# Kernel optimization log

Hardware: AMD Instinct MI355X
Metric: run time of the kernel (lower is better)

The kernel has to match this reference:

```python
import jax, jax.numpy as jnp
import numpy as np

B, T, D, H, S = 32, 2048, 512, 64, 3  # batch, time, feature_dim, flow hidden, flow steps
NBLK = 2  # nflows MADE default num_blocks
LOG_2PI = np.float32(np.log(2.0 * np.pi))


def setup_inputs() -> dict:
    key = jax.random.key(0)
    ks = jax.random.split(key, 20)
    rn = lambda k, sh: jax.random.normal(k, sh, dtype=jnp.float32) * 0.05
    return {
        "trend": rn(ks[0], (B, T)),
        "seasonal": rn(ks[1], (B, T)),
        "residual": rn(ks[2], (B, T)),
        # Linear(1, D) for trend / seasonal
        "Wt": rn(ks[3], (D, 1)), "bt": rn(ks[4], (D,)),
        "Ws": rn(ks[5], (D, 1)), "bs": rn(ks[6], (D,)),
        # per-flow-step MADE params (stacked over S steps). With features=1 the
        # masked initial layer contributes only its bias.
        "b_init": rn(ks[7], (S, H)),
        "Wc0": rn(ks[8], (S, H, 1)), "bc0": rn(ks[9], (S, H)),
        # two residual blocks per step: lin1, lin2, context gate
        "W1": rn(ks[10], (S, NBLK, H, H)), "b1": rn(ks[11], (S, NBLK, H)),
        "W2": rn(ks[12], (S, NBLK, H, H)), "b2": rn(ks[13], (S, NBLK, H)),
        "Wcb": rn(ks[14], (S, NBLK, H, 1)), "bcb": rn(ks[15], (S, NBLK, H)),
        # final Linear(H, 2): (unconstrained_scale, shift)
        "Wf": rn(ks[16], (S, 2, H)), "bf": rn(ks[17], (S, 2)),
    }


def _flow_log_prob(x, c, b_init, Wc0, bc0, W1, b1, W2, b2, Wcb, bcb, Wf, bf):
    # x: [N] residual values, c: [N,1] context (previous residual)
    z = x
    logdet = jnp.zeros_like(x)
    for i in range(S):
        h = c @ Wc0[i].T + (bc0[i] + b_init[i])  # [N,H]; input path is fully masked (features=1)
        for j in range(NBLK):  # MaskedResidualBlock
            t = jax.nn.relu(h) @ W1[i, j].T + b1[i, j]
            t = jax.nn.relu(t) @ W2[i, j].T + b2[i, j]
            g = c @ Wcb[i, j].T + bcb[i, j]
            h = h + t * jax.nn.sigmoid(g)  # F.glu(cat(t, g))
        out = jax.nn.relu(h) @ Wf[i].T + bf[i]  # [N,2]
        scale = jax.nn.softplus(out[:, 0]) + 1e-3
        z = scale * z + out[:, 1]
        logdet = logdet + jnp.log(scale)
    return -0.5 * z * z - 0.5 * LOG_2PI + logdet  # StandardNormal.log_prob + logabsdet


def reference(trend, seasonal, residual, Wt, bt, Ws, bs, b_init, Wc0, bc0,
              W1, b1, W2, b2, Wcb, bcb, Wf, bf):
    # Linear(1, D): y = x * W[:,0] + b
    feat_trend = trend[..., None] * Wt[:, 0] + bt      # [B,T,D]
    feat_seasonal = seasonal[..., None] * Ws[:, 0] + bs  # [B,T,D]
    x = residual.reshape(-1)                            # [B*T]
    prev = jnp.concatenate([jnp.zeros_like(residual[:, :1]), residual[:, :-1]], axis=1)
    c = prev.reshape(-1, 1)                             # [B*T,1]
    lp = _flow_log_prob(x, c, b_init, Wc0, bc0, W1, b1, W2, b2, Wcb, bcb, Wf, bf)
    lp = jax.lax.stop_gradient(lp).reshape(B, T, 1)     # torch.no_grad()
    return jnp.concatenate([feat_trend, feat_seasonal, lp], axis=-1)  # [B,T,2D+1]
```

## Files before the change

### kernel.cpp

```cpp
#include <hip/hip_runtime.h>

#define NB 32
#define NT 2048
#define ND 512
#define NH 64
#define NS 3
#define NBLKS 2
#define ROWLEN (2*ND + 1)

typedef __attribute__((ext_vector_type(8))) short bf16x8;
typedef float f32x4 __attribute__((ext_vector_type(4)));

#define W1_OFF 0
#define W2_OFF 24576
#define WF_OFF 49152
#define WS_ELEMS 52224

__device__ __forceinline__ unsigned int f2bf(float f) {
    unsigned int u = __float_as_uint(f);
    return (u + 0x7FFFu + ((u >> 16) & 1u)) >> 16;
}
__device__ __forceinline__ unsigned int pack2(float a, float b) {
    return f2bf(a) | (f2bf(b) << 16);
}

__global__ __launch_bounds__(256) void prepack(
    const float* __restrict__ W1, const float* __restrict__ W2,
    const float* __restrict__ Wf, unsigned short* __restrict__ ws)
{
    int idx = blockIdx.x * 256 + threadIdx.x;
    if (idx < 24576) {
        ws[W1_OFF + idx] = (unsigned short)f2bf(W1[idx]);
    } else if (idx < 49152) {
        int o = idx - 24576;
        ws[W2_OFF + o] = (unsigned short)f2bf(W2[o]);
    } else if (idx < WS_ELEMS) {
        int o = idx - 49152;
        int s = o >> 10, row = (o >> 6) & 15, m = o & 63;
        float v = (row < 2) ? Wf[s * 128 + row * 64 + m] : 0.0f;
        ws[WF_OFF + o] = (unsigned short)f2bf(v);
    }
}

__global__ __launch_bounds__(256, 4) void nf_main(
    const float* __restrict__ trend, const float* __restrict__ seasonal,
    const float* __restrict__ residual,
    const float* __restrict__ Wt, const float* __restrict__ bt,
    const float* __restrict__ Ws, const float* __restrict__ bs,
    const float* __restrict__ b_init, const float* __restrict__ Wc0,
    const float* __restrict__ bc0,
    const float* __restrict__ b1, const float* __restrict__ b2,
    const float* __restrict__ Wcb, const float* __restrict__ bcb,
    const float* __restrict__ bf_, const unsigned short* __restrict__ wpk,
    float* __restrict__ out)
{
    __shared__ float s_tr[64], s_se[64];
    __shared__ unsigned short s_X[4][16][72];

    const int tid  = threadIdx.x;
    const int row0 = blockIdx.x * 64;

    if (tid < 64) { s_tr[tid] = trend[row0 + tid]; s_se[tid] = seasonal[row0 + tid]; }
    __syncthreads();

    {
        float wv[4], bv[4];
        #pragma unroll
        for (int j = 0; j < 4; ++j) {
            int cc = tid + 256 * j;
            if (cc < ND) { wv[j] = Wt[cc];      bv[j] = bt[cc]; }
            else         { wv[j] = Ws[cc - ND]; bv[j] = bs[cc - ND]; }
        }
        for (int rr = 0; rr < 64; ++rr) {
            float a = s_tr[rr], sv = s_se[rr];
            float* rp = out + (size_t)(row0 + rr) * ROWLEN;
            #pragma unroll
            for (int j = 0; j < 4; ++j) {
                int cc = tid + 256 * j;
                rp[cc] = fmaf((cc < ND) ? a : sv, wv[j], bv[j]);
            }
        }
    }

    const int lane = tid & 63;
    const int wv_  = tid >> 6;
    const int r    = lane & 15;
    const int q    = lane >> 4;
    const int n    = row0 + wv_ * 16 + r;
    const float x  = residual[n];
    const float c  = ((n & (NT - 1)) == 0) ? 0.0f : residual[n - 1];
    unsigned short (* const X)[72] = s_X[wv_];
    const int u0 = 4 * q;

    float z = x, logdet = 0.0f;

    for (int i = 0; i < NS; ++i) {
        float h[4][4];
        #pragma unroll
        for (int t = 0; t < 4; ++t) {
            const int ub = i * NH + 16 * t + u0;
            const f32x4 wc  = *(const f32x4*)(Wc0 + ub);
            const f32x4 b0v = *(const f32x4*)(bc0 + ub);
            const f32x4 biv = *(const f32x4*)(b_init + ub);
            #pragma unroll
            for (int e = 0; e < 4; ++e) h[t][e] = fmaf(c, wc[e], b0v[e] + biv[e]);
        }

        for (int j = 0; j < NBLKS; ++j) {
            const int ij = i * NBLKS + j;
            #pragma unroll
            for (int t = 0; t < 4; ++t) {
                uint2 p;
                p.x = pack2(fmaxf(h[t][0], 0.f), fmaxf(h[t][1], 0.f));
                p.y = pack2(fmaxf(h[t][2], 0.f), fmaxf(h[t][3], 0.f));
                *(uint2*)&X[r][16 * t + u0] = p;
            }
            __syncthreads();

            f32x4 D[4];
            {
                const unsigned short* Wb = wpk + W1_OFF + ij * 4096;
                bf16x8 bA = *(const bf16x8*)&X[r][8 * q];
                bf16x8 bB = *(const bf16x8*)&X[r][32 + 8 * q];
                #pragma unroll
                for (int t = 0; t < 4; ++t) {
                    bf16x8 a0 = *(const bf16x8*)&Wb[(16 * t + r) * 64 + 8 * q];
                    bf16x8 a1 = *(const bf16x8*)&Wb[(16 * t + r) * 64 + 32 + 8 * q];
                    f32x4 d = {0.f, 0.f, 0.f, 0.f};
                    d = __builtin_amdgcn_mfma_f32_16x16x32_bf16(a0, bA, d, 0, 0, 0);
                    d = __builtin_amdgcn_mfma_f32_16x16x32_bf16(a1, bB, d, 0, 0, 0);
                    D[t] = d;
                }
            }
            #pragma unroll
            for (int t = 0; t < 4; ++t) {
                const f32x4 bb = *(const f32x4*)(b1 + ij * NH + 16 * t + u0);
                uint2 p;
                p.x = pack2(fmaxf(D[t][0] + bb[0], 0.f), fmaxf(D[t][1] + bb[1], 0.f));
                p.y = pack2(fmaxf(D[t][2] + bb[2], 0.f), fmaxf(D[t][3] + bb[3], 0.f));
                *(uint2*)&X[r][16 * t + u0] = p;
            }
            __syncthreads();

            {
                const unsigned short* Wb = wpk + W2_OFF + ij * 4096;
                bf16x8 bA = *(const bf16x8*)&X[r][8 * q];
                bf16x8 bB = *(const bf16x8*)&X[r][32 + 8 * q];
                #pragma unroll
                for (int t = 0; t < 4; ++t) {
                    bf16x8 a0 = *(const bf16x8*)&Wb[(16 * t + r) * 64 + 8 * q];
                    bf16x8 a1 = *(const bf16x8*)&Wb[(16 * t + r) * 64 + 32 + 8 * q];
                    f32x4 d = {0.f, 0.f, 0.f, 0.f};
                    d = __builtin_amdgcn_mfma_f32_16x16x32_bf16(a0, bA, d, 0, 0, 0);
                    d = __builtin_amdgcn_mfma_f32_16x16x32_bf16(a1, bB, d, 0, 0, 0);
                    D[t] = d;
                }
            }
            #pragma unroll
            for (int t = 0; t < 4; ++t) {
                const int ub = ij * NH + 16 * t + u0;
                const f32x4 b2v = *(const f32x4*)(b2 + ub);
                const f32x4 wg  = *(const f32x4*)(Wcb + ub);
                const f32x4 bg  = *(const f32x4*)(bcb + ub);
                #pragma unroll
                for (int e = 0; e < 4; ++e) {
                    float g  = fmaf(c, wg[e], bg[e]);
                    float sg = 1.0f / (1.0f + __expf(-g));
                    h[t][e] += (D[t][e] + b2v[e]) * sg;
                }
            }
        }

        #pragma unroll
        for (int t = 0; t < 4; ++t) {
            uint2 p;
            p.x = pack2(fmaxf(h[t][0], 0.f), fmaxf(h[t][1], 0.f));
            p.y = pack2(fmaxf(h[t][2], 0.f), fmaxf(h[t][3], 0.f));
            *(uint2*)&X[r][16 * t + u0] = p;
        }
        __syncthreads();
        {
            const unsigned short* Wb = wpk + WF_OFF + i * 1024;
            bf16x8 bA = *(const bf16x8*)&X[r][8 * q];
            bf16x8 bB = *(const bf16x8*)&X[r][32 + 8 * q];
            bf16x8 a0 = *(const bf16x8*)&Wb[r * 64 + 8 * q];
            bf16x8 a1 = *(const bf16x8*)&Wb[r * 64 + 32 + 8 * q];
            f32x4 d = {0.f, 0.f, 0.f, 0.f};
            d = __builtin_amdgcn_mfma_f32_16x16x32_bf16(a0, bA, d, 0, 0, 0);
            d = __builtin_amdgcn_mfma_f32_16x16x32_bf16(a1, bB, d, 0, 0, 0);
            float o0 = d[0] + bf_[2 * i];
            float o1 = d[1] + bf_[2 * i + 1];
            float sp = log1pf(__expf(o0)) + 1e-3f;
            z = fmaf(sp, z, o1);
            logdet += __logf(sp);
        }
        __syncthreads();
    }

    if (q == 0)
        out[(size_t)n * ROWLEN + 2 * ND] = fmaf(-0.5f, z * z, logdet) - 0.91893853320467274178f;
}

extern "C" void kernel_launch(void* const* d_in, const int* in_sizes, int n_in,
                              void* d_out, int out_size, void* d_ws, size_t ws_size,
                              hipStream_t stream) {
    const float* trend    = (const float*)d_in[0];
    const float* seasonal = (const float*)d_in[1];
    const float* residual = (const float*)d_in[2];
    const float* Wt       = (const float*)d_in[3];
    const float* bt       = (const float*)d_in[4];
    const float* Ws       = (const float*)d_in[5];
    const float* bs       = (const float*)d_in[6];
    const float* b_init   = (const float*)d_in[7];
    const float* Wc0      = (const float*)d_in[8];
    const float* bc0      = (const float*)d_in[9];
    const float* W1       = (const float*)d_in[10];
    const float* b1       = (const float*)d_in[11];
    const float* W2       = (const float*)d_in[12];
    const float* b2       = (const float*)d_in[13];
    const float* Wcb      = (const float*)d_in[14];
    const float* bcb      = (const float*)d_in[15];
    const float* Wf       = (const float*)d_in[16];
    const float* bfin     = (const float*)d_in[17];
    float* out            = (float*)d_out;
    unsigned short* wpk   = (unsigned short*)d_ws;

    hipLaunchKernelGGL(prepack, dim3(WS_ELEMS / 256), dim3(256), 0, stream, W1, W2, Wf, wpk);

    const int nrows = NB * NT;
    hipLaunchKernelGGL(nf_main, dim3(nrows / 64), dim3(256), 0, stream,
                       trend, seasonal, residual, Wt, bt, Ws, bs,
                       b_init, Wc0, bc0, b1, b2, Wcb, bcb, bfin, wpk, out);
}
```

Baseline: 355.3 us.

## Replace block barriers with wave-level syncs and move feature writes after flow

Each wave only touches its own slice of the shared staging buffer, so the block-wide __syncthreads are replaced with wavefront-scoped fences and wave barriers, and extra wave syncs guard the write-after-read hazards. The Linear(1,D) feature write moves from a block-level loop staged through shared memory to a per-wave loop after the flow computation. That loop broadcasts each row's trend and seasonal value with readlane, so the feature stores can overlap other waves' MFMA work. The launch-bounds occupancy hint drops from 4 to 2, which may raise register use. The feature-weight arrays grow to 16 registers per lane.

```diff
diff --git a/kernel.cpp b/kernel.cpp
--- a/kernel.cpp
+++ b/kernel.cpp
@@ -22,6 +22,16 @@
 }
 __device__ __forceinline__ unsigned int pack2(float a, float b) {
     return f2bf(a) | (f2bf(b) << 16);
+}
+
+__device__ __forceinline__ void wave_sync() {
+    __builtin_amdgcn_fence(__ATOMIC_ACQ_REL, "wavefront");
+    __builtin_amdgcn_wave_barrier();
+    __builtin_amdgcn_fence(__ATOMIC_ACQ_REL, "wavefront");
+}
+
+__device__ __forceinline__ float bcast(float v, int l) {
+    return __int_as_float(__builtin_amdgcn_readlane(__float_as_int(v), l));
 }
 
 __global__ __launch_bounds__(256) void prepack(
@@ -42,7 +52,7 @@
     }
 }
 
-__global__ __launch_bounds__(256, 4) void nf_main(
+__global__ __launch_bounds__(256, 2) void nf_main(
     const float* __restrict__ trend, const float* __restrict__ seasonal,
     const float* __restrict__ residual,
     const float* __restrict__ Wt, const float* __restrict__ bt,
@@ -54,41 +64,21 @@
     const float* __restrict__ bf_, const unsigned short* __restrict__ wpk,
     float* __restrict__ out)
 {
-    __shared__ float s_tr[64], s_se[64];
     __shared__ unsigned short s_X[4][16][72];
 
     const int tid  = threadIdx.x;
     const int row0 = blockIdx.x * 64;
-
-    if (tid < 64) { s_tr[tid] = trend[row0 + tid]; s_se[tid] = seasonal[row0 + tid]; }
-    __syncthreads();
-
-    {
-        float wv[4], bv[4];
-        #pragma unroll
-        for (int j = 0; j < 4; ++j) {
-            int cc = tid + 256 * j;
-            if (cc < ND) { wv[j] = Wt[cc];      bv[j] = bt[cc]; }
-            else         { wv[j] = Ws[cc - ND]; bv[j] = bs[cc - ND]; }
-        }
-        for (int rr = 0; rr < 64; ++rr) {
-            float a = s_tr[rr], sv = s_se[rr];
-            float* rp = out + (size_t)(row0 + rr) * ROWLEN;
-            #pragma unroll
-            for (int j = 0; j < 4; ++j) {
-                int cc = tid + 256 * j;
-                rp[cc] = fmaf((cc < ND) ? a : sv, wv[j], bv[j]);
-            }
-        }
-    }
-
     const int lane = tid & 63;
     const int wv_  = tid >> 6;
     const int r    = lane & 15;
     const int q    = lane >> 4;
     const int n    = row0 + wv_ * 16 + r;
-    const float x  = residual[n];
-    const float c  = ((n & (NT - 1)) == 0) ? 0.0f : residual[n - 1];
+
+    const float x   = residual[n];
+    const float c   = ((n & (NT - 1)) == 0) ? 0.0f : residual[n - 1];
+    const float trv = trend[n];
+    const float sev = seasonal[n];
+
     unsigned short (* const X)[72] = s_X[wv_];
     const int u0 = 4 * q;
 
@@ -115,7 +105,7 @@
                 p.y = pack2(fmaxf(h[t][2], 0.f), fmaxf(h[t][3], 0.f));
                 *(uint2*)&X[r][16 * t + u0] = p;
             }
-            __syncthreads();
+            wave_sync();
 
             f32x4 D[4];
             {
@@ -132,6 +122,7 @@
                     D[t] = d;
                 }
             }
+            wave_sync();
             #pragma unroll
             for (int t = 0; t < 4; ++t) {
                 const f32x4 bb = *(const f32x4*)(b1 + ij * NH + 16 * t + u0);
@@ -140,7 +131,7 @@
                 p.y = pack2(fmaxf(D[t][2] + bb[2], 0.f), fmaxf(D[t][3] + bb[3], 0.f));
                 *(uint2*)&X[r][16 * t + u0] = p;
             }
-            __syncthreads();
+            wave_sync();
 
             {
                 const unsigned short* Wb = wpk + W2_OFF + ij * 4096;
@@ -169,6 +160,7 @@
                     h[t][e] += (D[t][e] + b2v[e]) * sg;
                 }
             }
+            wave_sync();
         }
 
         #pragma unroll
@@ -178,7 +170,7 @@
             p.y = pack2(fmaxf(h[t][2], 0.f), fmaxf(h[t][3], 0.f));
             *(uint2*)&X[r][16 * t + u0] = p;
         }
-        __syncthreads();
+        wave_sync();
         {
             const unsigned short* Wb = wpk + WF_OFF + i * 1024;
             bf16x8 bA = *(const bf16x8*)&X[r][8 * q];
@@ -194,11 +186,29 @@
             z = fmaf(sp, z, o1);
             logdet += __logf(sp);
         }
-        __syncthreads();
+        wave_sync();
     }
 
     if (q == 0)
         out[(size_t)n * ROWLEN + 2 * ND] = fmaf(-0.5f, z * z, logdet) - 0.91893853320467274178f;
+
+    float wv[16], bv[16];
+    #pragma unroll
+    for (int j = 0; j < 16; ++j) {
+        const int cc = lane + 64 * j;
+        wv[j] = (j < 8) ? Wt[cc] : Ws[cc - ND];
+        bv[j] = (j < 8) ? bt[cc] : bs[cc - ND];
+    }
+    const int rbase = row0 + wv_ * 16;
+    #pragma unroll
+    for (int j = 0; j < 16; ++j) {
+        const int cc = lane + 64 * j;
+        const float src = (j < 8) ? trv : sev;
+        #pragma unroll
+        for (int rr = 0; rr < 16; ++rr) {
+            out[(size_t)(rbase + rr) * ROWLEN + cc] = fmaf(bcast(src, rr), wv[j], bv[j]);
+        }
+    }
 }
 
 extern "C" void kernel_launch(void* const* d_in, const int* in_sizes, int n_in,
@@ -225,7 +235,8 @@
     float* out            = (float*)d_out;
     unsigned short* wpk   = (unsigned short*)d_ws;
 
-    hipLaunchKernelGGL(prepack, dim3(WS_ELEMS / 256), dim3(256), 0, stream, W1, W2, Wf, wpk);
+    hipLaunchKernelGGL(prepack, dim3((WS_ELEMS + 255) / 256), dim3(256), 0, stream,
+                       W1, W2, Wf, wpk);
 
     const int nrows = NB * NT;
     hipLaunchKernelGGL(nf_main, dim3(nrows / 64), dim3(256), 0, stream,
```

After: 362.6 us. +2.0%, slower.
